# Kernel optimization log

Hardware: AMD Instinct MI355X
Metric: run time of the kernel (lower is better)

The kernel has to match this reference:

```python
import math
import jax, jax.numpy as jnp
import numpy as np

DIM = 128
NUM_PROJ = 256
ENC = jnp.asarray(2 ** np.arange(8), dtype=jnp.uint8)  # [1,2,4,...,128]
DEQUANT_SCALE = math.sqrt(math.pi / 2) / NUM_PROJ


def quantize_packed(x, S):
    # x: (..., dim) float32 -> packed uint8 (..., ceil(num_proj/8))
    projected = jnp.einsum('...d,pd->...p', x, S)
    signs = projected > 0  # bool (..., num_proj)
    pad_len = (-NUM_PROJ) % 8
    if pad_len > 0:
        pad = [(0, 0)] * (signs.ndim - 1) + [(0, pad_len)]
        signs = jnp.pad(signs, pad, constant_values=False)
    signs = signs.reshape(*signs.shape[:-1], -1, 8)  # (..., nbytes, 8)
    packed = jnp.sum(signs.astype(jnp.uint8) * ENC, axis=-1, dtype=jnp.uint8)
    return packed


def unpack_signs(packed):
    # packed: uint8 (..., nbytes) -> {-1,+1} float32 (..., num_proj)
    bits = jnp.bitwise_and(packed[..., None], ENC) > 0  # (..., nbytes, 8)
    bits = bits.reshape(*packed.shape[:-1], -1)[..., :NUM_PROJ]
    return bits.astype(jnp.float32) * 2.0 - 1.0


def setup_inputs() -> dict:
    key = jax.random.key(0)
    k1, k2, k3 = jax.random.split(key, 3)
    query = jax.random.normal(k1, (2, 32, 4096, DIM), dtype=jnp.float32)
    key_t = jax.random.normal(k2, (2, 32, 4096, DIM), dtype=jnp.float32)
    S = jax.random.normal(k3, (NUM_PROJ, DIM), dtype=jnp.float32)
    return {"query": query, "key": key_t, "S": S}


def reference(query, key, S):
    # quantize keys to bit-packed sign sketch, then estimate <query, key>
    packed = quantize_packed(key, S)                       # uint8 (..., 32)
    signs = unpack_signs(packed)                           # (..., 256)
    q_proj = jnp.einsum('...d,pd->...p', query, S)         # (..., 256)
    est = DEQUANT_SCALE * jnp.sum(q_proj * signs, axis=-1) # (B,H,S)
    return est
```

## Files before the change

kernel.cpp:

```cpp
#include <hip/hip_runtime.h>
#include <stdint.h>

#define DIM 128
#define NPROJ 256
#define TPB 128
#define TAU 0.035f
#define QCAP 512
#define DEQ 0.004895758348888673f

typedef _Float16 f16x8 __attribute__((ext_vector_type(8)));
typedef float f32x4 __attribute__((ext_vector_type(4)));

__global__ __launch_bounds__(256) void qjl_prep(const float* __restrict__ Sg,
                                                _Float16* __restrict__ ws) {
    int t = blockIdx.x * 256 + threadIdx.x;
    int lane = t & 63, fid = t >> 6;
    int f = fid & 1, ks = (fid >> 1) & 3, c = fid >> 3;
    int p = c * 32 + f * 16 + (lane & 15);
    int d0 = ks * 32 + (lane >> 4) * 8;
    const float4* s4 = (const float4*)(Sg + p * DIM + d0);
    float4 a = s4[0], b = s4[1];
    f16x8 h = {(_Float16)a.x, (_Float16)a.y, (_Float16)a.z, (_Float16)a.w,
               (_Float16)b.x, (_Float16)b.y, (_Float16)b.z, (_Float16)b.w};
    *(f16x8*)(ws + (size_t)fid * 512 + lane * 8) = h;
}

__global__ __launch_bounds__(256, 3) void qjl_main(
    const float* __restrict__ qg, const float* __restrict__ kg,
    const float* __restrict__ Sg, const _Float16* __restrict__ ws,
    float* __restrict__ out)
{
    __shared__ float    est_s[TPB];
    __shared__ uint32_t qmeta[QCAP];
    __shared__ float    qdlt[QCAP];
    __shared__ int      qn;

    const int tid = threadIdx.x, lane = tid & 63, wv = tid >> 6;
    const int m = lane & 15, quad = lane >> 4;
    const long tok0 = (long)blockIdx.x * TPB;
    if (tid == 0) qn = 0;
    __syncthreads();

    f16x8 ak[2][4], aq[2][4];
    #pragma unroll
    for (int rb = 0; rb < 2; ++rb) {
        long row = tok0 + wv * 32 + rb * 16 + m;
        const float* kr = kg + row * DIM;
        const float* qr = qg + row * DIM;
        #pragma unroll
        for (int ks = 0; ks < 4; ++ks) {
            int d0 = ks * 32 + quad * 8;
            float4 x = *(const float4*)(kr + d0);
            float4 y = *(const float4*)(kr + d0 + 4);
            ak[rb][ks] = (f16x8){(_Float16)x.x, (_Float16)x.y, (_Float16)x.z, (_Float16)x.w,
                                 (_Float16)y.x, (_Float16)y.y, (_Float16)y.z, (_Float16)y.w};
            float4 u = *(const float4*)(qr + d0);
            float4 v = *(const float4*)(qr + d0 + 4);
            aq[rb][ks] = (f16x8){(_Float16)u.x, (_Float16)u.y, (_Float16)u.z, (_Float16)u.w,
                                 (_Float16)v.x, (_Float16)v.y, (_Float16)v.z, (_Float16)v.w};
        }
    }

    float est[8] = {0.f, 0.f, 0.f, 0.f, 0.f, 0.f, 0.f, 0.f};

    for (int c = 0; c < 8; ++c) {
        f16x8 b0[4], b1[4];
        #pragma unroll
        for (int ks = 0; ks < 4; ++ks) {
            b0[ks] = *(const f16x8*)(ws + (size_t)(c * 8 + ks * 2 + 0) * 512 + lane * 8);
            b1[ks] = *(const f16x8*)(ws + (size_t)(c * 8 + ks * 2 + 1) * 512 + lane * 8);
        }
        #pragma unroll
        for (int rb = 0; rb < 2; ++rb) {
            f32x4 kacc0 = {0,0,0,0}, kacc1 = {0,0,0,0};
            f32x4 qacc0 = {0,0,0,0}, qacc1 = {0,0,0,0};
            #pragma unroll
            for (int ks = 0; ks < 4; ++ks) {
                kacc0 = __builtin_amdgcn_mfma_f32_16x16x32_f16(ak[rb][ks], b0[ks], kacc0, 0, 0, 0);
                kacc1 = __builtin_amdgcn_mfma_f32_16x16x32_f16(ak[rb][ks], b1[ks], kacc1, 0, 0, 0);
                qacc0 = __builtin_amdgcn_mfma_f32_16x16x32_f16(aq[rb][ks], b0[ks], qacc0, 0, 0, 0);
                qacc1 = __builtin_amdgcn_mfma_f32_16x16x32_f16(aq[rb][ks], b1[ks], qacc1, 0, 0, 0);
            }
            #pragma unroll
            for (int r = 0; r < 4; ++r) {
                int tl = wv * 32 + rb * 16 + quad * 4 + r;
                {
                    float kv = kacc0[r], qv = qacc0[r];
                    float sg = (kv > 0.f) ? 1.f : -1.f;
                    est[rb * 4 + r] += qv * sg;
                    if (fabsf(kv) < TAU) {
                        int p = c * 32 + m;
                        int idx = atomicAdd(&qn, 1);
                        if (idx < QCAP) {
                            qmeta[idx] = (uint32_t)tl | ((uint32_t)p << 8) | ((kv > 0.f ? 1u : 0u) << 16);
                            qdlt[idx]  = DEQ * qv * sg;
                        }
                    }
                }
                {
                    float kv = kacc1[r], qv = qacc1[r];
                    float sg = (kv > 0.f) ? 1.f : -1.f;
                    est[rb * 4 + r] += qv * sg;
                    if (fabsf(kv) < TAU) {
                        int p = c * 32 + 16 + m;
                        int idx = atomicAdd(&qn, 1);
                        if (idx < QCAP) {
                            qmeta[idx] = (uint32_t)tl | ((uint32_t)p << 8) | ((kv > 0.f ? 1u : 0u) << 16);
                            qdlt[idx]  = DEQ * qv * sg;
                        }
                    }
                }
            }
        }
    }

    #pragma unroll
    for (int rb = 0; rb < 2; ++rb) {
        #pragma unroll
        for (int r = 0; r < 4; ++r) {
            float e = est[rb * 4 + r];
            e += __shfl_xor(e, 1);
            e += __shfl_xor(e, 2);
            e += __shfl_xor(e, 4);
            e += __shfl_xor(e, 8);
            if (m == 0) est_s[wv * 32 + rb * 16 + quad * 4 + r] = DEQ * e;
        }
    }
    __syncthreads();

    int nc = qn < QCAP ? qn : QCAP;
    for (int i = wv; i < nc; i += 4) {
        uint32_t mm = qmeta[i];
        int tl = mm & 255;
        int p  = (mm >> 8) & 255;
        int sf = (mm >> 16) & 1;
        const float2* kr = (const float2*)(kg + (tok0 + tl) * DIM);
        const float2* sr = (const float2*)(Sg + (long)p * DIM);
        float2 ka = kr[lane], sa = sr[lane];
        double acc = (double)ka.x * (double)sa.x + (double)ka.y * (double)sa.y;
        acc += __shfl_xor(acc, 1);
        acc += __shfl_xor(acc, 2);
        acc += __shfl_xor(acc, 4);
        acc += __shfl_xor(acc, 8);
        acc += __shfl_xor(acc, 16);
        acc += __shfl_xor(acc, 32);
        int st = (acc > 0.0) ? 1 : 0;
        if (lane == 0 && st != sf) atomicAdd(&est_s[tl], -2.f * qdlt[i]);
    }
    __syncthreads();

    if (tid < TPB) out[tok0 + tid] = est_s[tid];
}

extern "C" void kernel_launch(void* const* d_in, const int* in_sizes, int n_in,
                              void* d_out, int out_size, void* d_ws, size_t ws_size,
                              hipStream_t stream) {
    const float* q = (const float*)d_in[0];
    const float* k = (const float*)d_in[1];
    const float* S = (const float*)d_in[2];
    float* out = (float*)d_out;
    _Float16* ws = (_Float16*)d_ws;
    hipLaunchKernelGGL(qjl_prep, dim3(16), dim3(256), 0, stream, S, ws);
    int nblocks = out_size / TPB;
    hipLaunchKernelGGL(qjl_main, dim3(nblocks), dim3(256), 0, stream, q, k, S, ws, out);
}
```

Baseline: 346.5 us.

## Prefetch projection fragments, shrink borderline threshold, per-thread fix-up dot products

Double-buffers the fp16 projection-matrix fragments in registers so the next chunk's loads overlap the current chunk's MFMAs. It also fully unrolls the chunk loop and lowers the near-zero threshold that marks projections for exact fp64 re-checking, which cuts the number of queued fix-ups. The fix-up pass now gives each thread one whole 128-element dot product instead of spreading it across a wavefront with shuffles. A smaller threshold raises the risk that fp16 rounding flips a sign that is never corrected, and the extra prefetch registers may reduce occupancy.

```diff
diff --git a/kernel.cpp b/kernel.cpp
--- a/kernel.cpp
+++ b/kernel.cpp
@@ -4,7 +4,7 @@
 #define DIM 128
 #define NPROJ 256
 #define TPB 128
-#define TAU 0.035f
+#define TAU 0.016f
 #define QCAP 512
 #define DEQ 0.004895758348888673f
 
@@ -41,6 +41,13 @@
     if (tid == 0) qn = 0;
     __syncthreads();
 
+    f16x8 bb[2][8];
+    #pragma unroll
+    for (int ks = 0; ks < 4; ++ks) {
+        bb[0][ks * 2 + 0] = *(const f16x8*)(ws + (size_t)(0 * 8 + ks * 2 + 0) * 512 + lane * 8);
+        bb[0][ks * 2 + 1] = *(const f16x8*)(ws + (size_t)(0 * 8 + ks * 2 + 1) * 512 + lane * 8);
+    }
+
     f16x8 ak[2][4], aq[2][4];
     #pragma unroll
     for (int rb = 0; rb < 2; ++rb) {
@@ -63,12 +70,15 @@
 
     float est[8] = {0.f, 0.f, 0.f, 0.f, 0.f, 0.f, 0.f, 0.f};
 
+    #pragma unroll
     for (int c = 0; c < 8; ++c) {
-        f16x8 b0[4], b1[4];
-        #pragma unroll
-        for (int ks = 0; ks < 4; ++ks) {
-            b0[ks] = *(const f16x8*)(ws + (size_t)(c * 8 + ks * 2 + 0) * 512 + lane * 8);
-            b1[ks] = *(const f16x8*)(ws + (size_t)(c * 8 + ks * 2 + 1) * 512 + lane * 8);
+        const int cur = c & 1;
+        if (c < 7) {
+            #pragma unroll
+            for (int ks = 0; ks < 4; ++ks) {
+                bb[cur ^ 1][ks * 2 + 0] = *(const f16x8*)(ws + (size_t)((c + 1) * 8 + ks * 2 + 0) * 512 + lane * 8);
+                bb[cur ^ 1][ks * 2 + 1] = *(const f16x8*)(ws + (size_t)((c + 1) * 8 + ks * 2 + 1) * 512 + lane * 8);
+            }
         }
         #pragma unroll
         for (int rb = 0; rb < 2; ++rb) {
@@ -76,10 +86,10 @@
             f32x4 qacc0 = {0,0,0,0}, qacc1 = {0,0,0,0};
             #pragma unroll
             for (int ks = 0; ks < 4; ++ks) {
-                kacc0 = __builtin_amdgcn_mfma_f32_16x16x32_f16(ak[rb][ks], b0[ks], kacc0, 0, 0, 0);
-                kacc1 = __builtin_amdgcn_mfma_f32_16x16x32_f16(ak[rb][ks], b1[ks], kacc1, 0, 0, 0);
-                qacc0 = __builtin_amdgcn_mfma_f32_16x16x32_f16(aq[rb][ks], b0[ks], qacc0, 0, 0, 0);
-                qacc1 = __builtin_amdgcn_mfma_f32_16x16x32_f16(aq[rb][ks], b1[ks], qacc1, 0, 0, 0);
+                kacc0 = __builtin_amdgcn_mfma_f32_16x16x32_f16(ak[rb][ks], bb[cur][ks * 2 + 0], kacc0, 0, 0, 0);
+                kacc1 = __builtin_amdgcn_mfma_f32_16x16x32_f16(ak[rb][ks], bb[cur][ks * 2 + 1], kacc1, 0, 0, 0);
+                qacc0 = __builtin_amdgcn_mfma_f32_16x16x32_f16(aq[rb][ks], bb[cur][ks * 2 + 0], qacc0, 0, 0, 0);
+                qacc1 = __builtin_amdgcn_mfma_f32_16x16x32_f16(aq[rb][ks], bb[cur][ks * 2 + 1], qacc1, 0, 0, 0);
             }
             #pragma unroll
             for (int r = 0; r < 4; ++r) {
@@ -88,7 +98,7 @@
                     float kv = kacc0[r], qv = qacc0[r];
                     float sg = (kv > 0.f) ? 1.f : -1.f;
                     est[rb * 4 + r] += qv * sg;
-                    if (fabsf(kv) < TAU) {
+                    if (__builtin_expect(fabsf(kv) < TAU, 0)) {
                         int p = c * 32 + m;
                         int idx = atomicAdd(&qn, 1);
                         if (idx < QCAP) {
@@ -101,7 +111,7 @@
                     float kv = kacc1[r], qv = qacc1[r];
                     float sg = (kv > 0.f) ? 1.f : -1.f;
                     est[rb * 4 + r] += qv * sg;
-                    if (fabsf(kv) < TAU) {
+                    if (__builtin_expect(fabsf(kv) < TAU, 0)) {
                         int p = c * 32 + 16 + m;
                         int idx = atomicAdd(&qn, 1);
                         if (idx < QCAP) {
@@ -129,23 +139,22 @@
     __syncthreads();
 
     int nc = qn < QCAP ? qn : QCAP;
-    for (int i = wv; i < nc; i += 4) {
+    for (int i = tid; i < nc; i += 256) {
         uint32_t mm = qmeta[i];
         int tl = mm & 255;
         int p  = (mm >> 8) & 255;
         int sf = (mm >> 16) & 1;
-        const float2* kr = (const float2*)(kg + (tok0 + tl) * DIM);
-        const float2* sr = (const float2*)(Sg + (long)p * DIM);
-        float2 ka = kr[lane], sa = sr[lane];
-        double acc = (double)ka.x * (double)sa.x + (double)ka.y * (double)sa.y;
-        acc += __shfl_xor(acc, 1);
-        acc += __shfl_xor(acc, 2);
-        acc += __shfl_xor(acc, 4);
-        acc += __shfl_xor(acc, 8);
-        acc += __shfl_xor(acc, 16);
-        acc += __shfl_xor(acc, 32);
+        const float4* kr = (const float4*)(kg + (tok0 + tl) * DIM);
+        const float4* sr = (const float4*)(Sg + (long)p * DIM);
+        double acc = 0.0;
+        #pragma unroll 8
+        for (int jj = 0; jj < 32; ++jj) {
+            float4 ka = kr[jj], sa = sr[jj];
+            acc += (double)ka.x * (double)sa.x + (double)ka.y * (double)sa.y
+                 + (double)ka.z * (double)sa.z + (double)ka.w * (double)sa.w;
+        }
         int st = (acc > 0.0) ? 1 : 0;
-        if (lane == 0 && st != sf) atomicAdd(&est_s[tl], -2.f * qdlt[i]);
+        if (st != sf) atomicAdd(&est_s[tl], -2.f * qdlt[i]);
     }
     __syncthreads();
 
```

Measured after the change: 450.5 us. 30.0% more time.
